# Kernel optimization log

Measured on AMD Instinct MI355X. Metric: run time of the kernel, lower is better.

The kernel has to match this reference:

```python
import jax, jax.numpy as jnp
import numpy as np

N = 50000      # num vertices
E = 600000     # num incidence pairs
M = 100000     # num hyperedges
IN = 256       # in_channels
H = 8          # heads
C = 32         # out_channels per head


def setup_inputs() -> dict:
    key = jax.random.key(0)
    k = jax.random.split(key, 5)
    X = jax.random.normal(k[0], (N, IN), jnp.float32)
    W = jax.random.normal(k[1], (IN, H * C), jnp.float32) * (1.0 / np.sqrt(IN))
    att_e = jax.random.normal(k[2], (1, H, C), jnp.float32) * 0.1
    vertex = jax.random.randint(k[3], (E,), 0, N)
    edges = jax.random.randint(k[4], (E,), 0, M)
    return {"X": X, "W": W, "att_e": att_e, "vertex": vertex, "edges": edges, "num_edges": M}


def reference(X, W, att_e, vertex, edges, num_edges):
    n, h, c = X.shape[0], att_e.shape[1], att_e.shape[2]
    X0 = X @ W                              # [N, H*C]
    Xh = X0.reshape(n, h, c)                # [N, H, C]
    Xve = Xh[vertex]                        # [E, H, C] gather node feats per incidence
    # mean-aggregate incidences -> hyperedge features
    cnt = jax.ops.segment_sum(jnp.ones((vertex.shape[0],), X.dtype), edges, num_segments=num_edges)
    Xe = jax.ops.segment_sum(Xve, edges, num_segments=num_edges) / jnp.maximum(cnt, 1.0)[:, None, None]  # [M, H, C]
    alpha_e = jnp.sum(Xe * att_e, axis=-1)  # [M, H]
    a_ev = alpha_e[edges]                   # [E, H]
    alpha = jnp.where(a_ev >= 0, a_ev, 0.2 * a_ev)  # leaky_relu(0.2)
    # numerically stable segment softmax over incidences grouped by vertex
    amax = jax.ops.segment_max(alpha, vertex, num_segments=n)[vertex]
    aexp = jnp.exp(alpha - amax)
    asum = jax.ops.segment_sum(aexp, vertex, num_segments=n)[vertex]
    attn = aexp / (asum + 1e-16)            # [E, H]
    Xev = Xe[edges] * attn[:, :, None]      # [E, H, C]
    Xv = jax.ops.segment_sum(Xev, vertex, num_segments=n)  # [N, H, C]
    return jax.nn.gelu(Xv.reshape(n, h * c), approximate=False)
```

## Files before the change

### kernel.cpp

```cpp
#include <hip/hip_runtime.h>
#include <hip/hip_bf16.h>
#include <math.h>

#define NV 50000
#define NE 600000
#define NM 100000
#define KIN 256
#define HCC 256
#define NHH 8

#define SCAN_NB0 25
#define SCAN_NB1 13

typedef unsigned int u32;
typedef unsigned short u16;
typedef _Float16 f16;
typedef _Float16 v8h __attribute__((ext_vector_type(8)));
typedef _Float16 v4h __attribute__((ext_vector_type(4)));
typedef float v4f __attribute__((ext_vector_type(4)));

__global__ __launch_bounds__(256) void k_gemm_f16(const float* __restrict__ X,
                                                  const float* __restrict__ W,
                                                  f16* __restrict__ X0) {
    __shared__ __align__(16) f16 sA[64][72];
    __shared__ __align__(16) f16 sB[64][72];
    const int t = threadIdx.x;
    const int r0 = blockIdx.x * 64;
    const int c0 = blockIdx.y * 64;
    const int wave = t >> 6;
    const int lane = t & 63;
    const int quad = lane >> 4;
    const int l16 = lane & 15;
    const int wr = wave & 1;
    const int wc = wave >> 1;

    v4f acc[2][2] = {{{0.f,0.f,0.f,0.f},{0.f,0.f,0.f,0.f}},
                     {{0.f,0.f,0.f,0.f},{0.f,0.f,0.f,0.f}}};

    for (int kc = 0; kc < KIN; kc += 64) {
        __syncthreads();
        #pragma unroll
        for (int i = 0; i < 4; ++i) {
            int lin = i * 256 + t;
            int row = lin >> 4;
            int k = (lin & 15) * 4;
            int gr = r0 + row;
            float4 x = make_float4(0.f, 0.f, 0.f, 0.f);
            if (gr < NV) x = *(const float4*)(X + (size_t)gr * KIN + kc + k);
            v4h hv = { (f16)x.x, (f16)x.y, (f16)x.z, (f16)x.w };
            *(v4h*)&sA[row][k] = hv;
        }
        #pragma unroll
        for (int i = 0; i < 4; ++i) {
            int lin = i * 256 + t;
            int k = lin >> 4;
            int n = (lin & 15) * 4;
            float4 b = *(const float4*)(W + (size_t)(kc + k) * HCC + c0 + n);
            sB[n + 0][k] = (f16)b.x;
            sB[n + 1][k] = (f16)b.y;
            sB[n + 2][k] = (f16)b.z;
            sB[n + 3][k] = (f16)b.w;
        }
        __syncthreads();
        #pragma unroll
        for (int ks = 0; ks < 2; ++ks) {
            const int kb = ks * 32 + quad * 8;
            v8h a[2], b[2];
            #pragma unroll
            for (int rf = 0; rf < 2; ++rf)
                a[rf] = *(const v8h*)&sA[wr * 32 + rf * 16 + l16][kb];
            #pragma unroll
            for (int cf = 0; cf < 2; ++cf)
                b[cf] = *(const v8h*)&sB[wc * 32 + cf * 16 + l16][kb];
            #pragma unroll
            for (int rf = 0; rf < 2; ++rf)
                #pragma unroll
                for (int cf = 0; cf < 2; ++cf)
                    acc[rf][cf] = __builtin_amdgcn_mfma_f32_16x16x32_f16(a[rf], b[cf], acc[rf][cf], 0, 0, 0);
        }
    }
    #pragma unroll
    for (int rf = 0; rf < 2; ++rf)
        #pragma unroll
        for (int cf = 0; cf < 2; ++cf)
            #pragma unroll
            for (int r = 0; r < 4; ++r) {
                int grow = r0 + wr * 32 + rf * 16 + quad * 4 + r;
                if (grow < NV)
                    X0[(size_t)grow * HCC + c0 + wc * 32 + cf * 16 + l16] = (f16)acc[rf][cf][r];
            }
}

__global__ __launch_bounds__(256) void k_count(const int* __restrict__ vertex,
                                               const int* __restrict__ edges,
                                               int* __restrict__ e_start,
                                               int* __restrict__ v_start) {
    int i = blockIdx.x * 256 + threadIdx.x;
    if (i >= NE) return;
    atomicAdd(e_start + edges[i] + 1, 1);
    atomicAdd(v_start + vertex[i] + 1, 1);
}

__global__ __launch_bounds__(1024) void k_scan_blk(int* __restrict__ a0,
                                                   int* __restrict__ a1,
                                                   int* __restrict__ bsum) {
    const int b = blockIdx.x;
    int* a;
    int n, base;
    if (b < SCAN_NB0) { a = a0; n = NM + 1; base = b * 4096; }
    else              { a = a1; n = NV + 1; base = (b - SCAN_NB0) * 4096; }
    const int t = threadIdx.x;
    const int lane = t & 63, w = t >> 6;
    const int i = base + t * 4;
    int4 v = make_int4(0, 0, 0, 0);
    if (i + 3 < n) v = *(const int4*)(a + i);
    else if (i < n) {
        v.x = a[i];
        if (i + 1 < n) v.y = a[i + 1];
        if (i + 2 < n) v.z = a[i + 2];
    }
    v.y += v.x; v.z += v.y; v.w += v.z;
    int s = v.w;
    #pragma unroll
    for (int d = 1; d < 64; d <<= 1) {
        int x = __shfl_up(s, d, 64);
        if (lane >= d) s += x;
    }
    __shared__ int partials[16];
    __shared__ int woff[16];
    if (lane == 63) partials[w] = s;
    __syncthreads();
    if (t < 16) {
        int p = partials[t];
        int ps = p;
        #pragma unroll
        for (int d = 1; d < 16; d <<= 1) {
            int x = __shfl_up(ps, d, 64);
            if (t >= d) ps += x;
        }
        woff[t] = ps - p;
        if (t == 15) bsum[b] = ps;
    }
    __syncthreads();
    const int add = (s - v.w) + woff[w];
    v.x += add; v.y += add; v.z += add; v.w += add;
    if (i + 3 < n) *(int4*)(a + i) = v;
    else if (i < n) {
        a[i] = v.x;
        if (i + 1 < n) a[i + 1] = v.y;
        if (i + 2 < n) a[i + 2] = v.z;
    }
}

__global__ __launch_bounds__(1024) void k_scan_add(int* __restrict__ a0, int* __restrict__ cur0,
                                                   int* __restrict__ a1, int* __restrict__ cur1,
                                                   const int* __restrict__ bsum) {
    const int b = blockIdx.x;
    int *a, *cur;
    int n, ncur, bs0, blocal;
    if (b < SCAN_NB0) { a = a0; cur = cur0; n = NM + 1; ncur = NM; bs0 = 0;        blocal = b; }
    else              { a = a1; cur = cur1; n = NV + 1; ncur = NV; bs0 = SCAN_NB0; blocal = b - SCAN_NB0; }
    const int t = threadIdx.x;
    const int lane = t & 63;
    int x = (lane < blocal) ? bsum[bs0 + lane] : 0;
    #pragma unroll
    for (int d = 1; d < 64; d <<= 1) x += __shfl_xor(x, d, 64);
    const int off = x;
    const int i = blocal * 4096 + t * 4;
    int4 v = make_int4(0, 0, 0, 0);
    if (i + 3 < n) {
        v = *(const int4*)(a + i);
        v.x += off; v.y += off; v.z += off; v.w += off;
        *(int4*)(a + i) = v;
    } else if (i < n) {
        v.x = a[i] + off; a[i] = v.x;
        if (i + 1 < n) { v.y = a[i + 1] + off; a[i + 1] = v.y; }
        if (i + 2 < n) { v.z = a[i + 2] + off; a[i + 2] = v.z; }
    }
    if (i + 3 < ncur) {
        *(int4*)(cur + i) = v;
    } else if (i < ncur) {
        cur[i] = v.x;
        if (i + 1 < ncur) cur[i + 1] = v.y;
        if (i + 2 < ncur) cur[i + 2] = v.z;
    }
}

__global__ __launch_bounds__(256) void k_fill(const int* __restrict__ vertex,
                                              const int* __restrict__ edges,
                                              int* __restrict__ e_cursor,
                                              int* __restrict__ v_cursor,
                                              int* __restrict__ e_list,
                                              int* __restrict__ v_list) {
    int i = blockIdx.x * 256 + threadIdx.x;
    if (i >= NE) return;
    int v = vertex[i], m = edges[i];
    int se = atomicAdd(e_cursor + m, 1);
    e_list[se] = v;
    int sv = atomicAdd(v_cursor + v, 1);
    v_list[sv] = m;
}

__global__ __launch_bounds__(256) void k_edge_gather(const int* __restrict__ e_start,
                                                     const int* __restrict__ e_list,
                                                     const f16* __restrict__ X0,
                                                     const float* __restrict__ att,
                                                     f16* __restrict__ Xe,
                                                     float* __restrict__ alpha_e) {
    int m = blockIdx.x * 4 + (threadIdx.x >> 6);
    int lane = threadIdx.x & 63;
    int s0 = e_start[m], s1 = e_start[m + 1];
    int c = lane * 4;
    float4 acc = make_float4(0.f, 0.f, 0.f, 0.f);
    int i = s0;
    for (; i + 3 < s1; i += 4) {
        int v0 = e_list[i], v1 = e_list[i + 1], v2 = e_list[i + 2], v3 = e_list[i + 3];
        v4h x0 = *(const v4h*)(X0 + (size_t)v0 * HCC + c);
        v4h x1 = *(const v4h*)(X0 + (size_t)v1 * HCC + c);
        v4h x2 = *(const v4h*)(X0 + (size_t)v2 * HCC + c);
        v4h x3 = *(const v4h*)(X0 + (size_t)v3 * HCC + c);
        acc.x += (float)x0[0] + (float)x1[0] + (float)x2[0] + (float)x3[0];
        acc.y += (float)x0[1] + (float)x1[1] + (float)x2[1] + (float)x3[1];
        acc.z += (float)x0[2] + (float)x1[2] + (float)x2[2] + (float)x3[2];
        acc.w += (float)x0[3] + (float)x1[3] + (float)x2[3] + (float)x3[3];
    }
    for (; i < s1; ++i) {
        int v0 = e_list[i];
        v4h x0 = *(const v4h*)(X0 + (size_t)v0 * HCC + c);
        acc.x += (float)x0[0];
        acc.y += (float)x0[1];
        acc.z += (float)x0[2];
        acc.w += (float)x0[3];
    }
    float inv = 1.0f / fmaxf((float)(s1 - s0), 1.0f);
    acc.x *= inv; acc.y *= inv; acc.z *= inv; acc.w *= inv;
    v4h xev = { (f16)acc.x, (f16)acc.y, (f16)acc.z, (f16)acc.w };
    *(v4h*)(Xe + (size_t)m * HCC + c) = xev;
    float4 av = *(const float4*)(att + c);
    float p = acc.x * av.x + acc.y * av.y + acc.z * av.z + acc.w * av.w;
    p += __shfl_xor(p, 1, 64);
    p += __shfl_xor(p, 2, 64);
    p += __shfl_xor(p, 4, 64);
    if ((lane & 7) == 0) alpha_e[m * NHH + (lane >> 3)] = p;
}

__global__ __launch_bounds__(256) void k_vertex_gather(const int* __restrict__ v_start,
                                                       const int* __restrict__ v_list,
                                                       const f16* __restrict__ Xe,
                                                       const float* __restrict__ alpha_e,
                                                       float* __restrict__ out) {
    int v = blockIdx.x * 4 + (threadIdx.x >> 6);
    int lane = threadIdx.x & 63;
    int s0 = v_start[v], s1 = v_start[v + 1];
    int h = lane >> 3;
    int c = lane * 4;
    float4 acc = make_float4(0.f, 0.f, 0.f, 0.f);
    float se = 0.f;
    int i = s0;
    for (; i + 1 < s1; i += 2) {
        int m0 = v_list[i], m1 = v_list[i + 1];
        float a0 = alpha_e[m0 * NHH + h];
        float a1 = alpha_e[m1 * NHH + h];
        v4h x0 = *(const v4h*)(Xe + (size_t)m0 * HCC + c);
        v4h x1 = *(const v4h*)(Xe + (size_t)m1 * HCC + c);
        a0 = (a0 >= 0.f) ? a0 : 0.2f * a0;
        a1 = (a1 >= 0.f) ? a1 : 0.2f * a1;
        float e0 = __expf(a0);
        float e1 = __expf(a1);
        acc.x += e0 * (float)x0[0] + e1 * (float)x1[0];
        acc.y += e0 * (float)x0[1] + e1 * (float)x1[1];
        acc.z += e0 * (float)x0[2] + e1 * (float)x1[2];
        acc.w += e0 * (float)x0[3] + e1 * (float)x1[3];
        se += e0 + e1;
    }
    if (i < s1) {
        int m0 = v_list[i];
        float a0 = alpha_e[m0 * NHH + h];
        v4h x0 = *(const v4h*)(Xe + (size_t)m0 * HCC + c);
        a0 = (a0 >= 0.f) ? a0 : 0.2f * a0;
        float e0 = __expf(a0);
        acc.x += e0 * (float)x0[0];
        acc.y += e0 * (float)x0[1];
        acc.z += e0 * (float)x0[2];
        acc.w += e0 * (float)x0[3];
        se += e0;
    }
    float inv = 1.0f / (se + 1e-16f);
    float4 o;
    float xx;
    xx = acc.x * inv; o.x = 0.5f * xx * (1.f + erff(xx * 0.70710678118f));
    xx = acc.y * inv; o.y = 0.5f * xx * (1.f + erff(xx * 0.70710678118f));
    xx = acc.z * inv; o.z = 0.5f * xx * (1.f + erff(xx * 0.70710678118f));
    xx = acc.w * inv; o.w = 0.5f * xx * (1.f + erff(xx * 0.70710678118f));
    *(float4*)(out + (size_t)v * HCC + c) = o;
}

extern "C" void kernel_launch(void* const* d_in, const int* in_sizes, int n_in,
                              void* d_out, int out_size, void* d_ws, size_t ws_size,
                              hipStream_t stream) {
    const float* X = (const float*)d_in[0];
    const float* W = (const float*)d_in[1];
    const float* att = (const float*)d_in[2];
    const int* vertex = (const int*)d_in[3];
    const int* edges = (const int*)d_in[4];
    float* out = (float*)d_out;

    char* ws = (char*)d_ws;
    size_t off = 0;
    #define WS_TAKE(bytes) (ws + off); off += (((size_t)(bytes)) + 15) & ~(size_t)15
    f16* X0 = (f16*)WS_TAKE((size_t)NV * HCC * 2);
    f16* Xe = (f16*)WS_TAKE((size_t)NM * HCC * 2);
    float* alpha_e = (float*)WS_TAKE((size_t)NM * NHH * 4);
    int* e_start = (int*)WS_TAKE((size_t)(NM + 1) * 4);
    int* v_start = (int*)WS_TAKE((size_t)(NV + 1) * 4);
    int* e_list = (int*)WS_TAKE((size_t)NE * 4);
    int* v_list = (int*)WS_TAKE((size_t)NE * 4);
    int* e_cursor = (int*)WS_TAKE((size_t)NM * 4);
    int* v_cursor = (int*)WS_TAKE((size_t)NV * 4);
    int* bsum = (int*)WS_TAKE(64 * 4);
    #undef WS_TAKE

    size_t hist_bytes = (((size_t)(NM + 1) * 4 + 15) & ~(size_t)15) +
                        (((size_t)(NV + 1) * 4 + 15) & ~(size_t)15);
    hipMemsetAsync(e_start, 0, hist_bytes, stream);

    const int EB = (NE + 255) / 256;
    k_count<<<EB, 256, 0, stream>>>(vertex, edges, e_start, v_start);
    k_scan_blk<<<SCAN_NB0 + SCAN_NB1, 1024, 0, stream>>>(e_start, v_start, bsum);
    k_scan_add<<<SCAN_NB0 + SCAN_NB1, 1024, 0, stream>>>(e_start, e_cursor, v_start, v_cursor, bsum);
    k_fill<<<EB, 256, 0, stream>>>(vertex, edges, e_cursor, v_cursor, e_list, v_list);
    dim3 ggrid((NV + 63) / 64, HCC / 64);
    k_gemm_f16<<<ggrid, 256, 0, stream>>>(X, W, X0);
    k_edge_gather<<<NM / 4, 256, 0, stream>>>(e_start, e_list, X0, att, Xe, alpha_e);
    k_vertex_gather<<<NV / 4, 256, 0, stream>>>(v_start, v_list, Xe, alpha_e, out);
}
```

Before: 398.1 us.

## Fuse count into GEMM launch and fill lists via recorded atomic ranks

The histogram count is merged into the GEMM kernel as extra blocks, and each atomic's return value is saved as a 16-bit rank per incidence. The fill step then writes CSR lists at start+rank with no second round of atomics, so the cursor arrays are dropped. The vertex-list fill is merged into the edge-gather launch. This removes kernel launches and one atomic pass and lets independent work overlap, at the cost of extra rank buffers. The fill order inside a segment now follows atomic order, which could change summation order.

```diff
diff --git a/kernel.cpp b/kernel.cpp
--- a/kernel.cpp
+++ b/kernel.cpp
@@ -12,6 +12,10 @@
 #define SCAN_NB0 25
 #define SCAN_NB1 13
 
+#define CNT_B 2344
+#define GEMM_BX 782
+#define GEMM_B (GEMM_BX * 4)
+
 typedef unsigned int u32;
 typedef unsigned short u16;
 typedef _Float16 f16;
@@ -19,14 +23,31 @@
 typedef _Float16 v4h __attribute__((ext_vector_type(4)));
 typedef float v4f __attribute__((ext_vector_type(4)));
 
-__global__ __launch_bounds__(256) void k_gemm_f16(const float* __restrict__ X,
-                                                  const float* __restrict__ W,
-                                                  f16* __restrict__ X0) {
+__global__ __launch_bounds__(256) void k_count_gemm(const int* __restrict__ vertex,
+                                                    const int* __restrict__ edges,
+                                                    int* __restrict__ e_hist,
+                                                    int* __restrict__ v_hist,
+                                                    u16* __restrict__ r_e,
+                                                    u16* __restrict__ r_v,
+                                                    const float* __restrict__ X,
+                                                    const float* __restrict__ W,
+                                                    f16* __restrict__ X0) {
     __shared__ __align__(16) f16 sA[64][72];
     __shared__ __align__(16) f16 sB[64][72];
+    const int bid = blockIdx.x;
     const int t = threadIdx.x;
-    const int r0 = blockIdx.x * 64;
-    const int c0 = blockIdx.y * 64;
+    if (bid < CNT_B) {
+        int i = bid * 256 + t;
+        if (i < NE) {
+            int v = vertex[i], m = edges[i];
+            r_e[i] = (u16)atomicAdd(e_hist + m + 1, 1);
+            r_v[i] = (u16)atomicAdd(v_hist + v + 1, 1);
+        }
+        return;
+    }
+    const int g = bid - CNT_B;
+    const int r0 = (g >> 2) * 64;
+    const int c0 = (g & 3) * 64;
     const int wave = t >> 6;
     const int lane = t & 63;
     const int quad = lane >> 4;
@@ -89,16 +110,6 @@
                 if (grow < NV)
                     X0[(size_t)grow * HCC + c0 + wc * 32 + cf * 16 + l16] = (f16)acc[rf][cf][r];
             }
-}
-
-__global__ __launch_bounds__(256) void k_count(const int* __restrict__ vertex,
-                                               const int* __restrict__ edges,
-                                               int* __restrict__ e_start,
-                                               int* __restrict__ v_start) {
-    int i = blockIdx.x * 256 + threadIdx.x;
-    if (i >= NE) return;
-    atomicAdd(e_start + edges[i] + 1, 1);
-    atomicAdd(v_start + vertex[i] + 1, 1);
 }
 
 __global__ __launch_bounds__(1024) void k_scan_blk(int* __restrict__ a0,
@@ -152,62 +163,65 @@
     }
 }
 
-__global__ __launch_bounds__(1024) void k_scan_add(int* __restrict__ a0, int* __restrict__ cur0,
-                                                   int* __restrict__ a1, int* __restrict__ cur1,
+__global__ __launch_bounds__(1024) void k_scan_add(int* __restrict__ a0,
+                                                   int* __restrict__ a1,
                                                    const int* __restrict__ bsum) {
     const int b = blockIdx.x;
-    int *a, *cur;
-    int n, ncur, bs0, blocal;
-    if (b < SCAN_NB0) { a = a0; cur = cur0; n = NM + 1; ncur = NM; bs0 = 0;        blocal = b; }
-    else              { a = a1; cur = cur1; n = NV + 1; ncur = NV; bs0 = SCAN_NB0; blocal = b - SCAN_NB0; }
+    int* a;
+    int n, bs0, blocal;
+    if (b < SCAN_NB0) { a = a0; n = NM + 1; bs0 = 0;        blocal = b; }
+    else              { a = a1; n = NV + 1; bs0 = SCAN_NB0; blocal = b - SCAN_NB0; }
     const int t = threadIdx.x;
     const int lane = t & 63;
     int x = (lane < blocal) ? bsum[bs0 + lane] : 0;
     #pragma unroll
     for (int d = 1; d < 64; d <<= 1) x += __shfl_xor(x, d, 64);
     const int off = x;
+    if (off == 0 && blocal == 0) {  }
     const int i = blocal * 4096 + t * 4;
-    int4 v = make_int4(0, 0, 0, 0);
     if (i + 3 < n) {
-        v = *(const int4*)(a + i);
+        int4 v = *(const int4*)(a + i);
         v.x += off; v.y += off; v.z += off; v.w += off;
         *(int4*)(a + i) = v;
     } else if (i < n) {
-        v.x = a[i] + off; a[i] = v.x;
-        if (i + 1 < n) { v.y = a[i + 1] + off; a[i + 1] = v.y; }
-        if (i + 2 < n) { v.z = a[i + 2] + off; a[i + 2] = v.z; }
-    }
-    if (i + 3 < ncur) {
-        *(int4*)(cur + i) = v;
-    } else if (i < ncur) {
-        cur[i] = v.x;
-        if (i + 1 < ncur) cur[i + 1] = v.y;
-        if (i + 2 < ncur) cur[i + 2] = v.z;
-    }
-}
-
-__global__ __launch_bounds__(256) void k_fill(const int* __restrict__ vertex,
-                                              const int* __restrict__ edges,
-                                              int* __restrict__ e_cursor,
-                                              int* __restrict__ v_cursor,
-                                              int* __restrict__ e_list,
-                                              int* __restrict__ v_list) {
+        a[i] += off;
+        if (i + 1 < n) a[i + 1] += off;
+        if (i + 2 < n) a[i + 2] += off;
+    }
+}
+
+__global__ __launch_bounds__(256) void k_efill(const int* __restrict__ vertex,
+                                               const int* __restrict__ edges,
+                                               const u16* __restrict__ r_e,
+                                               const int* __restrict__ e_start,
+                                               int* __restrict__ e_list) {
     int i = blockIdx.x * 256 + threadIdx.x;
     if (i >= NE) return;
-    int v = vertex[i], m = edges[i];
-    int se = atomicAdd(e_cursor + m, 1);
-    e_list[se] = v;
-    int sv = atomicAdd(v_cursor + v, 1);
-    v_list[sv] = m;
-}
-
-__global__ __launch_bounds__(256) void k_edge_gather(const int* __restrict__ e_start,
-                                                     const int* __restrict__ e_list,
-                                                     const f16* __restrict__ X0,
-                                                     const float* __restrict__ att,
-                                                     f16* __restrict__ Xe,
-                                                     float* __restrict__ alpha_e) {
-    int m = blockIdx.x * 4 + (threadIdx.x >> 6);
+    int m = edges[i];
+    e_list[e_start[m] + (int)r_e[i]] = vertex[i];
+}
+
+__global__ __launch_bounds__(256) void k_vfill_egather(const int* __restrict__ vertex,
+                                                       const int* __restrict__ edges,
+                                                       const u16* __restrict__ r_v,
+                                                       const int* __restrict__ v_start,
+                                                       int* __restrict__ v_list,
+                                                       const int* __restrict__ e_start,
+                                                       const int* __restrict__ e_list,
+                                                       const f16* __restrict__ X0,
+                                                       const float* __restrict__ att,
+                                                       f16* __restrict__ Xe,
+                                                       float* __restrict__ alpha_e) {
+    const int bid = blockIdx.x;
+    if (bid < CNT_B) {
+        int i = bid * 256 + threadIdx.x;
+        if (i < NE) {
+            int v = vertex[i];
+            v_list[v_start[v] + (int)r_v[i]] = edges[i];
+        }
+        return;
+    }
+    int m = (bid - CNT_B) * 4 + (threadIdx.x >> 6);
     int lane = threadIdx.x & 63;
     int s0 = e_start[m], s1 = e_start[m + 1];
     int c = lane * 4;
@@ -315,8 +329,8 @@
     int* v_start = (int*)WS_TAKE((size_t)(NV + 1) * 4);
     int* e_list = (int*)WS_TAKE((size_t)NE * 4);
     int* v_list = (int*)WS_TAKE((size_t)NE * 4);
-    int* e_cursor = (int*)WS_TAKE((size_t)NM * 4);
-    int* v_cursor = (int*)WS_TAKE((size_t)NV * 4);
+    u16* r_e = (u16*)WS_TAKE((size_t)NE * 2);
+    u16* r_v = (u16*)WS_TAKE((size_t)NE * 2);
     int* bsum = (int*)WS_TAKE(64 * 4);
     #undef WS_TAKE
 
@@ -324,13 +338,12 @@
                         (((size_t)(NV + 1) * 4 + 15) & ~(size_t)15);
     hipMemsetAsync(e_start, 0, hist_bytes, stream);
 
-    const int EB = (NE + 255) / 256;
-    k_count<<<EB, 256, 0, stream>>>(vertex, edges, e_start, v_start);
+    k_count_gemm<<<CNT_B + GEMM_B, 256, 0, stream>>>(vertex, edges, e_start, v_start,
+                                                     r_e, r_v, X, W, X0);
     k_scan_blk<<<SCAN_NB0 + SCAN_NB1, 1024, 0, stream>>>(e_start, v_start, bsum);
-    k_scan_add<<<SCAN_NB0 + SCAN_NB1, 1024, 0, stream>>>(e_start, e_cursor, v_start, v_cursor, bsum);
-    k_fill<<<EB, 256, 0, stream>>>(vertex, edges, e_cursor, v_cursor, e_list, v_list);
-    dim3 ggrid((NV + 63) / 64, HCC / 64);
-    k_gemm_f16<<<ggrid, 256, 0, stream>>>(X, W, X0);
-    k_edge_gather<<<NM / 4, 256, 0, stream>>>(e_start, e_list, X0, att, Xe, alpha_e);
+    k_scan_add<<<SCAN_NB0 + SCAN_NB1, 1024, 0, stream>>>(e_start, v_start, bsum);
+    k_efill<<<CNT_B, 256, 0, stream>>>(vertex, edges, r_e, e_start, e_list);
+    k_vfill_egather<<<CNT_B + NM / 4, 256, 0, stream>>>(vertex, edges, r_v, v_start, v_list,
+                                                        e_start, e_list, X0, att, Xe, alpha_e);
     k_vertex_gather<<<NV / 4, 256, 0, stream>>>(v_start, v_list, Xe, alpha_e, out);
 }
```

Result: faster. 318.8 us (-19.9%).
